# Performance work log

Hardware: AMD Instinct MI355X
Metric: run time of the kernel (lower is better)

Reference implementation:

```python
import jax, jax.numpy as jnp
import numpy as np

N_NODES = 100000
N_EDGES = 1600000
D_IN = 128
D_HID = 128
D_OUT = 64


def setup_inputs() -> dict:
    key = jax.random.key(0)
    ks = jax.random.split(key, 8)
    x = jax.random.normal(ks[0], (N_NODES, D_IN), dtype=jnp.float32)
    edge_index = jax.random.randint(ks[1], (2, N_EDGES), 0, N_NODES, dtype=jnp.int64)
    s1 = 1.0 / np.sqrt(D_IN)
    s2 = 1.0 / np.sqrt(D_HID)
    W1_l = jax.random.normal(ks[2], (D_IN, D_HID), dtype=jnp.float32) * s1
    W1_r = jax.random.normal(ks[3], (D_IN, D_HID), dtype=jnp.float32) * s1
    b1 = jnp.zeros((D_HID,), dtype=jnp.float32)
    W2_l = jax.random.normal(ks[4], (D_HID, D_OUT), dtype=jnp.float32) * s2
    W2_r = jax.random.normal(ks[5], (D_HID, D_OUT), dtype=jnp.float32) * s2
    b2 = jnp.zeros((D_OUT,), dtype=jnp.float32)
    return {"x": x, "edge_index": edge_index, "W1_l": W1_l, "b1": b1,
            "W1_r": W1_r, "W2_l": W2_l, "b2": b2, "W2_r": W2_r}


def _sage_conv(x, src, dst, Wl, bl, Wr, num_nodes):
    # PyG SAGEConv (aggr='mean', root_weight=True):
    #   out = lin_l(mean_{j in N(i)} x_j) + lin_r(x_i)
    agg = jax.ops.segment_sum(x[src], dst, num_segments=num_nodes)        # [N, d]
    deg = jax.ops.segment_sum(jnp.ones((src.shape[0],), dtype=x.dtype), dst,
                              num_segments=num_nodes)                      # [N]
    mean = agg / jnp.maximum(deg, 1.0)[:, None]
    return mean @ Wl + bl + x @ Wr


def reference(x, edge_index, W1_l, b1, W1_r, W2_l, b2, W2_r):
    src, dst = edge_index[0], edge_index[1]
    n = x.shape[0]
    h = jax.nn.relu(_sage_conv(x, src, dst, W1_l, b1, W1_r, n))
    # dropout is identity in eval mode
    out = _sage_conv(h, src, dst, W2_l, b2, W2_r, n)
    return jax.nn.log_softmax(out, axis=1)
```

## Files before the change

### kernel.cpp

```cpp
#include <hip/hip_runtime.h>
#include <math.h>

#define NN 100000
#define NE 1600000
#define SBN 512
#define NSB ((NN + SBN - 1) / SBN)
#define SBCAP 10240
#define EPB 8192
#define NBA ((NE + EPB - 1) / EPB)

typedef __attribute__((ext_vector_type(8))) short bf16x8;
typedef __attribute__((ext_vector_type(8))) unsigned short ush8;
typedef __attribute__((ext_vector_type(4))) float f32x4;

static __device__ __forceinline__ float b2f(unsigned short u) {
    return __uint_as_float(((unsigned int)u) << 16);
}
static __device__ __forceinline__ unsigned short f2bf(float f) {
    unsigned int u = __float_as_uint(f);
    u += 0x7fffu + ((u >> 16) & 1u);
    return (unsigned short)(u >> 16);
}

__global__ __launch_bounds__(256)
void k_cvt_x(const float* __restrict__ in, unsigned short* __restrict__ outb, long total8) {
    long i = (long)blockIdx.x * 256 + threadIdx.x;
    long stride = (long)gridDim.x * 256;
    for (; i < total8; i += stride) {
        const float4* p = (const float4*)(in + i * 8);
        float4 a = p[0], b = p[1];
        ush8 r;
        r[0] = f2bf(a.x); r[1] = f2bf(a.y); r[2] = f2bf(a.z); r[3] = f2bf(a.w);
        r[4] = f2bf(b.x); r[5] = f2bf(b.y); r[6] = f2bf(b.z); r[7] = f2bf(b.w);
        *(ush8*)(outb + i * 8) = r;
    }
}

__global__ __launch_bounds__(256)
void k_cvt_w(const float* __restrict__ W, unsigned short* __restrict__ Wt, int N) {
    int id = blockIdx.x * 256 + threadIdx.x;
    if (id < N * 128) {
        int n = id >> 7, k = id & 127;
        Wt[id] = f2bf(W[k * N + n]);
    }
}

__global__ __launch_bounds__(256)
void k_cvt_wcat(const float* __restrict__ W2l, const float* __restrict__ W2r,
                unsigned short* __restrict__ Wt) {
    int id = blockIdx.x * 256 + threadIdx.x;
    if (id < 128 * 128) {
        int n = id >> 7, k = id & 127;
        float v = (n < 64) ? W2l[k * 64 + n] : W2r[k * 64 + (n - 64)];
        Wt[id] = f2bf(v);
    }
}

__global__ __launch_bounds__(1024)
void k_binA(const int* __restrict__ src, const int* __restrict__ dst,
            int* __restrict__ gcnt, int* __restrict__ pairs) {
    __shared__ int lsort[EPB];
    __shared__ int lhist[256];
    __shared__ int lofs[256];
    __shared__ int lpos[NSB];
    __shared__ int gbase[NSB];
    const int tid = threadIdx.x;
    const int base = blockIdx.x * EPB;
    const int cnt = min(EPB, NE - base);

    int v[8], bn[8];
    #pragma unroll
    for (int k = 0; k < 8; ++k) {
        int i = k * 1024 + tid;
        if (i < cnt) {
            int d = dst[base + i], s = src[base + i];
            v[k] = (s << 9) | (d & 511);
            bn[k] = d >> 9;
        } else bn[k] = -1;
    }
    if (tid < 256) lhist[tid] = 0;
    __syncthreads();
    #pragma unroll
    for (int k = 0; k < 8; ++k) if (bn[k] >= 0) atomicAdd(&lhist[bn[k]], 1);
    __syncthreads();
    if (tid < 256) lofs[tid] = lhist[tid];
    __syncthreads();
    for (int d = 1; d < 256; d <<= 1) {
        int u = (tid < 256 && tid >= d) ? lofs[tid - d] : 0;
        __syncthreads();
        if (tid < 256) lofs[tid] += u;
        __syncthreads();
    }
    if (tid < 256) lofs[tid] -= lhist[tid];
    __syncthreads();
    if (tid < NSB) {
        lpos[tid] = lofs[tid];
        gbase[tid] = atomicAdd(&gcnt[tid], lhist[tid]);
    }
    __syncthreads();
    #pragma unroll
    for (int k = 0; k < 8; ++k) if (bn[k] >= 0) {
        int slot = atomicAdd(&lpos[bn[k]], 1);
        lsort[slot] = v[k];
    }
    __syncthreads();
    for (int i = tid; i < cnt; i += 1024) {
        int lo = 0, hi = NSB - 1;
        while (lo < hi) { int mid = (lo + hi + 1) >> 1; if (lofs[mid] <= i) lo = mid; else hi = mid - 1; }
        int off = gbase[lo] + (i - lofs[lo]);
        if (off < SBCAP)
            __builtin_nontemporal_store(lsort[i], &pairs[(size_t)lo * SBCAP + off]);
    }
}

__global__ __launch_bounds__(1024)
void k_sortB(const int* __restrict__ gcnt, int* __restrict__ pairs,
             int* __restrict__ offs, int* __restrict__ deg) {
    __shared__ int lstage[SBCAP];
    __shared__ int lhist[SBN], lscan[SBN], lpos[SBN];
    const int sb = blockIdx.x, tid = threadIdx.x;
    const int cnt = min(gcnt[sb], SBCAP);
    int* __restrict__ region = pairs + (size_t)sb * SBCAP;

    for (int i = tid; i < cnt; i += 1024) lstage[i] = region[i];
    if (tid < SBN) lhist[tid] = 0;
    __syncthreads();
    for (int i = tid; i < cnt; i += 1024) atomicAdd(&lhist[lstage[i] & 511], 1);
    __syncthreads();
    if (tid < SBN) lscan[tid] = lhist[tid];
    __syncthreads();
    for (int d = 1; d < SBN; d <<= 1) {
        int u = (tid < SBN && tid >= d) ? lscan[tid - d] : 0;
        __syncthreads();
        if (tid < SBN) lscan[tid] += u;
        __syncthreads();
    }
    if (tid < SBN) {
        int ex = lscan[tid] - lhist[tid];
        lpos[tid] = ex;
        int node = sb * SBN + tid;
        if (node < NN) { offs[node] = sb * SBCAP + ex; deg[node] = lhist[tid]; }
    }
    __syncthreads();
    for (int i = tid; i < cnt; i += 1024) {
        int val = lstage[i];
        int slot = atomicAdd(&lpos[val & 511], 1);
        region[slot] = val >> 9;
    }
}

__global__ __launch_bounds__(256)
void k_aggregate_bf(const unsigned short* __restrict__ feat, const int* __restrict__ csr,
                    const int* __restrict__ offs, const int* __restrict__ deg,
                    unsigned short* __restrict__ outmean) {
    const int wid = threadIdx.x >> 6, lane = threadIdx.x & 63;
    const int q = lane >> 4, l4 = lane & 15;
    const int node = blockIdx.x * 4 + wid;
    if (node >= NN) return;
    int off = __builtin_amdgcn_readfirstlane(offs[node]);
    int dg  = __builtin_amdgcn_readfirstlane(deg[node]);
    const ush8* __restrict__ f8 = (const ush8*)feat;
    float acc[8];
    #pragma unroll
    for (int i = 0; i < 8; ++i) acc[i] = 0.f;
    int j = 0;
    for (; j + 8 <= dg; j += 8) {
        int e0 = csr[off + j + q];
        int e1 = csr[off + j + 4 + q];
        ush8 v0 = f8[(size_t)e0 * 16 + l4];
        ush8 v1 = f8[(size_t)e1 * 16 + l4];
        #pragma unroll
        for (int i = 0; i < 8; ++i) acc[i] += b2f(v0[i]) + b2f(v1[i]);
    }
    for (; j + 4 <= dg; j += 4) {
        int e0 = csr[off + j + q];
        ush8 v0 = f8[(size_t)e0 * 16 + l4];
        #pragma unroll
        for (int i = 0; i < 8; ++i) acc[i] += b2f(v0[i]);
    }
    int rem = dg - j;
    if (q < rem) {
        int e0 = csr[off + j + q];
        ush8 v0 = f8[(size_t)e0 * 16 + l4];
        #pragma unroll
        for (int i = 0; i < 8; ++i) acc[i] += b2f(v0[i]);
    }
    #pragma unroll
    for (int i = 0; i < 8; ++i) {
        acc[i] += __shfl_xor(acc[i], 16);
        acc[i] += __shfl_xor(acc[i], 32);
    }
    if (q == 0) {
        float inv = 1.0f / (float)(dg > 0 ? dg : 1);
        ush8 r;
        #pragma unroll
        for (int i = 0; i < 8; ++i) r[i] = f2bf(acc[i] * inv);
        ((ush8*)outmean)[(size_t)node * 16 + l4] = r;
    }
}

template <int BN, bool RELU, bool OUTBF>
__global__ __launch_bounds__(256)
void k_gemm_mfma(const unsigned short* __restrict__ Am, const unsigned short* __restrict__ Ax,
                 const unsigned short* __restrict__ Wtl, const unsigned short* __restrict__ Wtr,
                 const float* __restrict__ bias, void* __restrict__ outp) {
    constexpr int BM = 128;
    constexpr int WAVES_N = BN / 64;
    constexpr int WAVES_M = 4 / WAVES_N;
    constexpr int MR = BM / (WAVES_M * 16);
    constexpr int NR = 4;
    __shared__ __align__(16) short As[BM * 40];
    __shared__ __align__(16) short Ws[BN * 40];

    const int tid = threadIdx.x;
    const int wave = tid >> 6, lane = tid & 63;
    const int l15 = lane & 15, kg = lane >> 4;
    const int wc = wave % WAVES_N, wr = wave / WAVES_N;
    const int rowbase = wr * MR * 16;
    const int colbase = wc * 64;
    const int row0 = blockIdx.x * BM;

    f32x4 acc[MR][NR];
    #pragma unroll
    for (int mr = 0; mr < MR; ++mr)
        #pragma unroll
        for (int nr = 0; nr < NR; ++nr) acc[mr][nr] = (f32x4){0.f, 0.f, 0.f, 0.f};

    for (int s = 0; s < 2; ++s) {
        const unsigned short* __restrict__ A  = s ? Ax : Am;
        const unsigned short* __restrict__ Wt = s ? Wtr : Wtl;
        for (int kc = 0; kc < 128; kc += 32) {
            __syncthreads();
            #pragma unroll
            for (int i = 0; i < (BM * 4) / 256; ++i) {
                int c = tid + 256 * i; int r = c >> 2, g = c & 3;
                ush8 v = {0, 0, 0, 0, 0, 0, 0, 0};
                int grow = row0 + r;
                if (grow < NN) v = *(const ush8*)&A[(size_t)grow * 128 + kc + g * 8];
                *(ush8*)&As[r * 40 + g * 8] = v;
            }
            #pragma unroll
            for (int i = 0; i < (BN * 4) / 256; ++i) {
                int c = tid + 256 * i; int n = c >> 2, g = c & 3;
                *(ush8*)&Ws[n * 40 + g * 8] = *(const ush8*)&Wt[n * 128 + kc + g * 8];
            }
            __syncthreads();
            bf16x8 af[MR], bfr[NR];
            #pragma unroll
            for (int mr = 0; mr < MR; ++mr)
                af[mr] = *(const bf16x8*)&As[(rowbase + mr * 16 + l15) * 40 + kg * 8];
            #pragma unroll
            for (int nr = 0; nr < NR; ++nr)
                bfr[nr] = *(const bf16x8*)&Ws[(colbase + nr * 16 + l15) * 40 + kg * 8];
            #pragma unroll
            for (int mr = 0; mr < MR; ++mr)
                #pragma unroll
                for (int nr = 0; nr < NR; ++nr)
                    acc[mr][nr] = __builtin_amdgcn_mfma_f32_16x16x32_bf16(
                        af[mr], bfr[nr], acc[mr][nr], 0, 0, 0);
        }
    }
    const int r4 = kg * 4;
    #pragma unroll
    for (int mr = 0; mr < MR; ++mr) {
        #pragma unroll
        for (int nr = 0; nr < NR; ++nr) {
            int col = colbase + nr * 16 + l15;
            float bv = bias[col];
            #pragma unroll
            for (int j = 0; j < 4; ++j) {
                int row = row0 + rowbase + mr * 16 + r4 + j;
                if (row < NN) {
                    float v = acc[mr][nr][j] + bv;
                    if (RELU) v = fmaxf(v, 0.f);
                    if (OUTBF) ((unsigned short*)outp)[(size_t)row * BN + col] = f2bf(v);
                    else       ((float*)outp)[(size_t)row * BN + col] = v;
                }
            }
        }
    }
}

__global__ __launch_bounds__(256)
void k_gemm_cat(const unsigned short* __restrict__ A, const unsigned short* __restrict__ Wt,
                const float* __restrict__ b2,
                unsigned short* __restrict__ g, unsigned short* __restrict__ z) {
    constexpr int BM = 128, BN = 128, MR = 4, NR = 4;
    __shared__ __align__(16) short As[BM * 40];
    __shared__ __align__(16) short Ws[BN * 40];

    const int tid = threadIdx.x;
    const int wave = tid >> 6, lane = tid & 63;
    const int l15 = lane & 15, kg = lane >> 4;
    const int wc = wave % 2, wr = wave / 2;
    const int rowbase = wr * MR * 16;
    const int colbase = wc * 64;
    const int row0 = blockIdx.x * BM;

    f32x4 acc[MR][NR];
    #pragma unroll
    for (int mr = 0; mr < MR; ++mr)
        #pragma unroll
        for (int nr = 0; nr < NR; ++nr) acc[mr][nr] = (f32x4){0.f, 0.f, 0.f, 0.f};

    for (int kc = 0; kc < 128; kc += 32) {
        __syncthreads();
        #pragma unroll
        for (int i = 0; i < 2; ++i) {
            int c = tid + 256 * i; int r = c >> 2, gg = c & 3;
            ush8 v = {0, 0, 0, 0, 0, 0, 0, 0};
            int grow = row0 + r;
            if (grow < NN) v = *(const ush8*)&A[(size_t)grow * 128 + kc + gg * 8];
            *(ush8*)&As[r * 40 + gg * 8] = v;
        }
        #pragma unroll
        for (int i = 0; i < 2; ++i) {
            int c = tid + 256 * i; int n = c >> 2, gg = c & 3;
            *(ush8*)&Ws[n * 40 + gg * 8] = *(const ush8*)&Wt[n * 128 + kc + gg * 8];
        }
        __syncthreads();
        bf16x8 af[MR], bfr[NR];
        #pragma unroll
        for (int mr = 0; mr < MR; ++mr)
            af[mr] = *(const bf16x8*)&As[(rowbase + mr * 16 + l15) * 40 + kg * 8];
        #pragma unroll
        for (int nr = 0; nr < NR; ++nr)
            bfr[nr] = *(const bf16x8*)&Ws[(colbase + nr * 16 + l15) * 40 + kg * 8];
        #pragma unroll
        for (int mr = 0; mr < MR; ++mr)
            #pragma unroll
            for (int nr = 0; nr < NR; ++nr)
                acc[mr][nr] = __builtin_amdgcn_mfma_f32_16x16x32_bf16(
                    af[mr], bfr[nr], acc[mr][nr], 0, 0, 0);
    }
    const int r4 = kg * 4;
    #pragma unroll
    for (int mr = 0; mr < MR; ++mr) {
        #pragma unroll
        for (int nr = 0; nr < NR; ++nr) {
            int col = colbase + nr * 16 + l15;
            float bv = (col >= 64) ? b2[col - 64] : 0.f;
            #pragma unroll
            for (int j = 0; j < 4; ++j) {
                int row = row0 + rowbase + mr * 16 + r4 + j;
                if (row < NN) {
                    float v = acc[mr][nr][j] + bv;
                    unsigned short bv16 = f2bf(v);
                    if (col < 64) g[(size_t)row * 64 + col] = bv16;
                    else          z[(size_t)row * 64 + (col - 64)] = bv16;
                }
            }
        }
    }
}

__global__ __launch_bounds__(256)
void k_agg_lsm(const unsigned short* __restrict__ gbuf, const unsigned short* __restrict__ zbuf,
               const int* __restrict__ csr, const int* __restrict__ offs,
               const int* __restrict__ deg, float* __restrict__ out) {
    const int wid = threadIdx.x >> 6, lane = threadIdx.x & 63;
    const int g8 = lane >> 3, l8 = lane & 7;
    const int node = blockIdx.x * 4 + wid;
    if (node >= NN) return;
    int off = __builtin_amdgcn_readfirstlane(offs[node]);
    int dg  = __builtin_amdgcn_readfirstlane(deg[node]);
    const ush8* __restrict__ f8 = (const ush8*)gbuf;
    float acc[8];
    #pragma unroll
    for (int i = 0; i < 8; ++i) acc[i] = 0.f;
    int j = 0;
    for (; j + 16 <= dg; j += 16) {
        int e0 = csr[off + j + g8];
        int e1 = csr[off + j + 8 + g8];
        ush8 v0 = f8[(size_t)e0 * 8 + l8];
        ush8 v1 = f8[(size_t)e1 * 8 + l8];
        #pragma unroll
        for (int i = 0; i < 8; ++i) acc[i] += b2f(v0[i]) + b2f(v1[i]);
    }
    for (; j + 8 <= dg; j += 8) {
        int e0 = csr[off + j + g8];
        ush8 v0 = f8[(size_t)e0 * 8 + l8];
        #pragma unroll
        for (int i = 0; i < 8; ++i) acc[i] += b2f(v0[i]);
    }
    int rem = dg - j;
    if (g8 < rem) {
        int e0 = csr[off + j + g8];
        ush8 v0 = f8[(size_t)e0 * 8 + l8];
        #pragma unroll
        for (int i = 0; i < 8; ++i) acc[i] += b2f(v0[i]);
    }
    #pragma unroll
    for (int i = 0; i < 8; ++i) {
        acc[i] += __shfl_xor(acc[i], 8);
        acc[i] += __shfl_xor(acc[i], 16);
        acc[i] += __shfl_xor(acc[i], 32);
    }
    float inv = 1.0f / (float)(dg > 0 ? dg : 1);
    ush8 zv = ((const ush8*)zbuf)[(size_t)node * 8 + l8];
    float v[8];
    float m = -1e30f;
    #pragma unroll
    for (int i = 0; i < 8; ++i) {
        v[i] = acc[i] * inv + b2f(zv[i]);
        m = fmaxf(m, v[i]);
    }
    #pragma unroll
    for (int d = 4; d >= 1; d >>= 1) m = fmaxf(m, __shfl_xor(m, d));
    float ss = 0.f;
    #pragma unroll
    for (int i = 0; i < 8; ++i) ss += __expf(v[i] - m);
    #pragma unroll
    for (int d = 4; d >= 1; d >>= 1) ss += __shfl_xor(ss, d);
    float lse = m + logf(ss);
    if (g8 == 0) {
        float4 o0 = make_float4(v[0] - lse, v[1] - lse, v[2] - lse, v[3] - lse);
        float4 o1 = make_float4(v[4] - lse, v[5] - lse, v[6] - lse, v[7] - lse);
        *(float4*)&out[(size_t)node * 64 + l8 * 8]     = o0;
        *(float4*)&out[(size_t)node * 64 + l8 * 8 + 4] = o1;
    }
}

extern "C" void kernel_launch(void* const* d_in, const int* in_sizes, int n_in,
                              void* d_out, int out_size, void* d_ws, size_t ws_size,
                              hipStream_t stream) {
    const float* x   = (const float*)d_in[0];
    const int* edges = (const int*)d_in[1];
    const float* W1l = (const float*)d_in[2];
    const float* b1  = (const float*)d_in[3];
    const float* W1r = (const float*)d_in[4];
    const float* W2l = (const float*)d_in[5];
    const float* b2  = (const float*)d_in[6];
    const float* W2r = (const float*)d_in[7];
    float* out = (float*)d_out;

    const int* src = edges;
    const int* dst = edges + NE;

    char* ws = (char*)d_ws;
    size_t o = 0;
    auto alloc = [&](size_t bytes) -> void* {
        void* p = ws + o;
        o = (o + bytes + 255) & ~(size_t)255;
        return p;
    };
    int* gcnt  = (int*)alloc((size_t)NSB * 4);
    int* pairs = (int*)alloc((size_t)NSB * SBCAP * 4);
    int* offs  = (int*)alloc((size_t)NN * 4);
    int* deg   = (int*)alloc((size_t)NN * 4);
    unsigned short* xb    = (unsigned short*)alloc((size_t)NN * 128 * 2);
    unsigned short* meanb = (unsigned short*)alloc((size_t)NN * 128 * 2);
    unsigned short* hb    = (unsigned short*)alloc((size_t)NN * 128 * 2);
    unsigned short* gbuf  = (unsigned short*)alloc((size_t)NN * 64 * 2);
    unsigned short* zbuf  = (unsigned short*)alloc((size_t)NN * 64 * 2);
    unsigned short* Wt1l  = (unsigned short*)alloc(128 * 128 * 2);
    unsigned short* Wt1r  = (unsigned short*)alloc(128 * 128 * 2);
    unsigned short* Wtcat = (unsigned short*)alloc(128 * 128 * 2);

    hipMemsetAsync(gcnt, 0, (size_t)NSB * 4, stream);

    k_cvt_x<<<2048, 256, 0, stream>>>(x, xb, (long)NN * 128 / 8);
    k_cvt_w<<<(128 * 128 + 255) / 256, 256, 0, stream>>>(W1l, Wt1l, 128);
    k_cvt_w<<<(128 * 128 + 255) / 256, 256, 0, stream>>>(W1r, Wt1r, 128);
    k_cvt_wcat<<<(128 * 128 + 255) / 256, 256, 0, stream>>>(W2l, W2r, Wtcat);

    k_binA<<<NBA, 1024, 0, stream>>>(src, dst, gcnt, pairs);
    k_sortB<<<NSB, 1024, 0, stream>>>(gcnt, pairs, offs, deg);

    const int GEMM_GRID = (NN + 127) / 128;
    k_aggregate_bf<<<(NN + 3) / 4, 256, 0, stream>>>(xb, pairs, offs, deg, meanb);
    k_gemm_mfma<128, true, true><<<GEMM_GRID, 256, 0, stream>>>(meanb, xb, Wt1l, Wt1r, b1, hb);
    k_gemm_cat<<<GEMM_GRID, 256, 0, stream>>>(hb, Wtcat, b2, gbuf, zbuf);
    k_agg_lsm<<<(NN + 3) / 4, 256, 0, stream>>>(gbuf, zbuf, pairs, offs, deg, out);
}
```

Measured before the change: 224.0 us.

## Fuse layer-1 neighbor mean aggregation into the MFMA GEMM kernel via LDS

Merges the first-layer gather/mean kernel with the dual GEMM. Each 128-row block aggregates its nodes' neighbor means into a swizzled 32KB LDS tile, then runs MFMA directly. The intermediate mean buffer and its global write/read round trip go away. The x-side A operand and the weights are now read straight from global memory with no LDS staging. The risk is lower parallelism during aggregation: 782 blocks of 4 waves, each looping over 32 nodes. The larger LDS footprint may also reduce occupancy.

```diff
diff --git a/kernel.cpp b/kernel.cpp
--- a/kernel.cpp
+++ b/kernel.cpp
@@ -150,75 +150,72 @@
 }
 
 __global__ __launch_bounds__(256)
-void k_aggregate_bf(const unsigned short* __restrict__ feat, const int* __restrict__ csr,
-                    const int* __restrict__ offs, const int* __restrict__ deg,
-                    unsigned short* __restrict__ outmean) {
-    const int wid = threadIdx.x >> 6, lane = threadIdx.x & 63;
-    const int q = lane >> 4, l4 = lane & 15;
-    const int node = blockIdx.x * 4 + wid;
-    if (node >= NN) return;
-    int off = __builtin_amdgcn_readfirstlane(offs[node]);
-    int dg  = __builtin_amdgcn_readfirstlane(deg[node]);
-    const ush8* __restrict__ f8 = (const ush8*)feat;
-    float acc[8];
-    #pragma unroll
-    for (int i = 0; i < 8; ++i) acc[i] = 0.f;
-    int j = 0;
-    for (; j + 8 <= dg; j += 8) {
-        int e0 = csr[off + j + q];
-        int e1 = csr[off + j + 4 + q];
-        ush8 v0 = f8[(size_t)e0 * 16 + l4];
-        ush8 v1 = f8[(size_t)e1 * 16 + l4];
-        #pragma unroll
-        for (int i = 0; i < 8; ++i) acc[i] += b2f(v0[i]) + b2f(v1[i]);
-    }
-    for (; j + 4 <= dg; j += 4) {
-        int e0 = csr[off + j + q];
-        ush8 v0 = f8[(size_t)e0 * 16 + l4];
-        #pragma unroll
-        for (int i = 0; i < 8; ++i) acc[i] += b2f(v0[i]);
-    }
-    int rem = dg - j;
-    if (q < rem) {
-        int e0 = csr[off + j + q];
-        ush8 v0 = f8[(size_t)e0 * 16 + l4];
-        #pragma unroll
-        for (int i = 0; i < 8; ++i) acc[i] += b2f(v0[i]);
-    }
-    #pragma unroll
-    for (int i = 0; i < 8; ++i) {
-        acc[i] += __shfl_xor(acc[i], 16);
-        acc[i] += __shfl_xor(acc[i], 32);
-    }
-    if (q == 0) {
-        float inv = 1.0f / (float)(dg > 0 ? dg : 1);
-        ush8 r;
-        #pragma unroll
-        for (int i = 0; i < 8; ++i) r[i] = f2bf(acc[i] * inv);
-        ((ush8*)outmean)[(size_t)node * 16 + l4] = r;
-    }
-}
-
-template <int BN, bool RELU, bool OUTBF>
-__global__ __launch_bounds__(256)
-void k_gemm_mfma(const unsigned short* __restrict__ Am, const unsigned short* __restrict__ Ax,
-                 const unsigned short* __restrict__ Wtl, const unsigned short* __restrict__ Wtr,
-                 const float* __restrict__ bias, void* __restrict__ outp) {
-    constexpr int BM = 128;
-    constexpr int WAVES_N = BN / 64;
-    constexpr int WAVES_M = 4 / WAVES_N;
-    constexpr int MR = BM / (WAVES_M * 16);
-    constexpr int NR = 4;
-    __shared__ __align__(16) short As[BM * 40];
-    __shared__ __align__(16) short Ws[BN * 40];
+void k_fused1(const unsigned short* __restrict__ xb, const int* __restrict__ csr,
+              const int* __restrict__ offs, const int* __restrict__ deg,
+              const unsigned short* __restrict__ Wtl, const unsigned short* __restrict__ Wtr,
+              const float* __restrict__ bias, unsigned short* __restrict__ hb) {
+    __shared__ short meanL[128 * 128];
 
     const int tid = threadIdx.x;
     const int wave = tid >> 6, lane = tid & 63;
+    const int row0 = blockIdx.x * 128;
+
+    {
+        const int q = lane >> 4, l4 = lane & 15;
+        const ush8* __restrict__ f8 = (const ush8*)xb;
+        for (int nl = wave; nl < 128; nl += 4) {
+            int node = row0 + nl;
+            float acc[8];
+            #pragma unroll
+            for (int i = 0; i < 8; ++i) acc[i] = 0.f;
+            int dg = 0;
+            if (node < NN) {
+                int off = __builtin_amdgcn_readfirstlane(offs[node]);
+                dg = __builtin_amdgcn_readfirstlane(deg[node]);
+                int j = 0;
+                for (; j + 8 <= dg; j += 8) {
+                    int e0 = csr[off + j + q];
+                    int e1 = csr[off + j + 4 + q];
+                    ush8 v0 = f8[(size_t)e0 * 16 + l4];
+                    ush8 v1 = f8[(size_t)e1 * 16 + l4];
+                    #pragma unroll
+                    for (int i = 0; i < 8; ++i) acc[i] += b2f(v0[i]) + b2f(v1[i]);
+                }
+                for (; j + 4 <= dg; j += 4) {
+                    int e0 = csr[off + j + q];
+                    ush8 v0 = f8[(size_t)e0 * 16 + l4];
+                    #pragma unroll
+                    for (int i = 0; i < 8; ++i) acc[i] += b2f(v0[i]);
+                }
+                int rem = dg - j;
+                if (q < rem) {
+                    int e0 = csr[off + j + q];
+                    ush8 v0 = f8[(size_t)e0 * 16 + l4];
+                    #pragma unroll
+                    for (int i = 0; i < 8; ++i) acc[i] += b2f(v0[i]);
+                }
+                #pragma unroll
+                for (int i = 0; i < 8; ++i) {
+                    acc[i] += __shfl_xor(acc[i], 16);
+                    acc[i] += __shfl_xor(acc[i], 32);
+                }
+            }
+            if (q == 0) {
+                float inv = 1.0f / (float)(dg > 0 ? dg : 1);
+                ush8 r;
+                #pragma unroll
+                for (int i = 0; i < 8; ++i) r[i] = f2bf(acc[i] * inv);
+                *(ush8*)&meanL[nl * 128 + (l4 ^ (nl & 7)) * 8] = r;
+            }
+        }
+    }
+    __syncthreads();
+
+    constexpr int MR = 4, NR = 4;
     const int l15 = lane & 15, kg = lane >> 4;
-    const int wc = wave % WAVES_N, wr = wave / WAVES_N;
-    const int rowbase = wr * MR * 16;
+    const int wc = wave % 2, wr = wave / 2;
+    const int rowbase = wr * 64;
     const int colbase = wc * 64;
-    const int row0 = blockIdx.x * BM;
 
     f32x4 acc[MR][NR];
     #pragma unroll
@@ -227,31 +224,25 @@
         for (int nr = 0; nr < NR; ++nr) acc[mr][nr] = (f32x4){0.f, 0.f, 0.f, 0.f};
 
     for (int s = 0; s < 2; ++s) {
-        const unsigned short* __restrict__ A  = s ? Ax : Am;
         const unsigned short* __restrict__ Wt = s ? Wtr : Wtl;
+        #pragma unroll
         for (int kc = 0; kc < 128; kc += 32) {
-            __syncthreads();
-            #pragma unroll
-            for (int i = 0; i < (BM * 4) / 256; ++i) {
-                int c = tid + 256 * i; int r = c >> 2, g = c & 3;
-                ush8 v = {0, 0, 0, 0, 0, 0, 0, 0};
-                int grow = row0 + r;
-                if (grow < NN) v = *(const ush8*)&A[(size_t)grow * 128 + kc + g * 8];
-                *(ush8*)&As[r * 40 + g * 8] = v;
+            bf16x8 af[MR], bfr[NR];
+            #pragma unroll
+            for (int mr = 0; mr < MR; ++mr) {
+                int rl = rowbase + mr * 16 + l15;
+                if (s == 0) {
+                    int slot = (kc >> 3) + kg;
+                    af[mr] = *(const bf16x8*)&meanL[rl * 128 + (slot ^ (rl & 7)) * 8];
+                } else {
+                    int grow = row0 + rl;
+                    if (grow >= NN) grow = NN - 1;
+                    af[mr] = *(const bf16x8*)&xb[(size_t)grow * 128 + kc + kg * 8];
+                }
             }
             #pragma unroll
-            for (int i = 0; i < (BN * 4) / 256; ++i) {
-                int c = tid + 256 * i; int n = c >> 2, g = c & 3;
-                *(ush8*)&Ws[n * 40 + g * 8] = *(const ush8*)&Wt[n * 128 + kc + g * 8];
-            }
-            __syncthreads();
-            bf16x8 af[MR], bfr[NR];
-            #pragma unroll
-            for (int mr = 0; mr < MR; ++mr)
-                af[mr] = *(const bf16x8*)&As[(rowbase + mr * 16 + l15) * 40 + kg * 8];
-            #pragma unroll
             for (int nr = 0; nr < NR; ++nr)
-                bfr[nr] = *(const bf16x8*)&Ws[(colbase + nr * 16 + l15) * 40 + kg * 8];
+                bfr[nr] = *(const bf16x8*)&Wt[(size_t)(colbase + nr * 16 + l15) * 128 + kc + kg * 8];
             #pragma unroll
             for (int mr = 0; mr < MR; ++mr)
                 #pragma unroll
@@ -271,10 +262,8 @@
             for (int j = 0; j < 4; ++j) {
                 int row = row0 + rowbase + mr * 16 + r4 + j;
                 if (row < NN) {
-                    float v = acc[mr][nr][j] + bv;
-                    if (RELU) v = fmaxf(v, 0.f);
-                    if (OUTBF) ((unsigned short*)outp)[(size_t)row * BN + col] = f2bf(v);
-                    else       ((float*)outp)[(size_t)row * BN + col] = v;
+                    float v = fmaxf(acc[mr][nr][j] + bv, 0.f);
+                    hb[(size_t)row * 128 + col] = f2bf(v);
                 }
             }
         }
@@ -449,7 +438,6 @@
     int* offs  = (int*)alloc((size_t)NN * 4);
     int* deg   = (int*)alloc((size_t)NN * 4);
     unsigned short* xb    = (unsigned short*)alloc((size_t)NN * 128 * 2);
-    unsigned short* meanb = (unsigned short*)alloc((size_t)NN * 128 * 2);
     unsigned short* hb    = (unsigned short*)alloc((size_t)NN * 128 * 2);
     unsigned short* gbuf  = (unsigned short*)alloc((size_t)NN * 64 * 2);
     unsigned short* zbuf  = (unsigned short*)alloc((size_t)NN * 64 * 2);
@@ -468,8 +456,7 @@
     k_sortB<<<NSB, 1024, 0, stream>>>(gcnt, pairs, offs, deg);
 
     const int GEMM_GRID = (NN + 127) / 128;
-    k_aggregate_bf<<<(NN + 3) / 4, 256, 0, stream>>>(xb, pairs, offs, deg, meanb);
-    k_gemm_mfma<128, true, true><<<GEMM_GRID, 256, 0, stream>>>(meanb, xb, Wt1l, Wt1r, b1, hb);
+    k_fused1<<<GEMM_GRID, 256, 0, stream>>>(xb, pairs, offs, deg, Wt1l, Wt1r, b1, hb);
     k_gemm_cat<<<GEMM_GRID, 256, 0, stream>>>(hb, Wtcat, b2, gbuf, zbuf);
     k_agg_lsm<<<(NN + 3) / 4, 256, 0, stream>>>(gbuf, zbuf, pairs, offs, deg, out);
 }
```

After: 329.9 us. +47.3%, slower.
